# Kernel tuning notes

Measured on AMD Instinct MI355X. Metric: run time of the kernel, lower is better.

Reference implementation:

```python
import jax, jax.numpy as jnp
import numpy as np

BS, N_OPS, N_JOBS, N_MA, E, H = 256, 2000, 50, 40, 128, 128


def setup_inputs() -> dict:
    key = jax.random.key(0)
    ks = jax.random.split(key, 12)
    return {
        "ops_emb": jax.random.normal(ks[0], (BS, N_OPS, E), jnp.float32),
        "ma_emb": jax.random.normal(ks[1], (BS, N_MA, E), jnp.float32),
        "next_op": jax.random.randint(ks[2], (BS, N_JOBS), 0, N_OPS),
        "action_mask": jnp.ones((BS, N_JOBS * N_MA + 1), dtype=bool),
        "dummy": jax.random.normal(ks[3], (2 * E,), jnp.float32),
        "W1": jax.random.normal(ks[4], (2 * E, H), jnp.float32) * 0.05,
        "b1": jax.random.normal(ks[5], (H,), jnp.float32) * 0.05,
        "W2": jax.random.normal(ks[6], (H, H), jnp.float32) * 0.05,
        "b2": jax.random.normal(ks[7], (H,), jnp.float32) * 0.05,
        "W3": jax.random.normal(ks[8], (H, 1), jnp.float32) * 0.05,
        "b3": jax.random.normal(ks[9], (1,), jnp.float32) * 0.05,
    }


def reference(ops_emb, ma_emb, next_op, action_mask, dummy, W1, b1, W2, b2, W3, b3):
    bs, n_ma = ma_emb.shape[:2]
    e = ma_emb.shape[-1]
    # gather_by_index: job_emb [bs, n_jobs, E]
    job_emb = jnp.take_along_axis(ops_emb, next_op[..., None], axis=1)
    # Fused broadcast-concat + first linear: cat(job, ma) @ W1 == job @ W1[:E] + ma @ W1[E:]
    Wj, Wm = W1[:e], W1[e:]
    job_proj = jnp.einsum("bje,eh->bjh", job_emb, Wj)  # [bs, n_jobs, H]
    ma_proj = jnp.einsum("bme,eh->bmh", ma_emb, Wm)    # [bs, n_ma, H]
    h1 = jax.nn.relu(job_proj[:, :, None, :] + ma_proj[:, None, :, :] + b1)  # [bs, nj, nm, H]
    h2 = jax.nn.relu(jnp.einsum("bjmh,hk->bjmk", h1, W2) + b2)
    pair_logits = (jnp.einsum("bjmh,ho->bjmo", h2, W3) + b3)[..., 0]  # [bs, nj, nm]
    pair_logits = pair_logits.reshape(bs, -1)
    # no-op logit from dummy vector through the same MLP
    d1 = jax.nn.relu(dummy @ W1 + b1)
    d2 = jax.nn.relu(d1 @ W2 + b2)
    noop = (d2 @ W3 + b3)  # [1]
    noop = jnp.broadcast_to(noop[None, :], (bs, 1))
    logits = jnp.concatenate([noop, pair_logits], axis=1)  # [bs, nj*nm+1]
    return logits, action_mask
```

## Files before the change

kernel.cpp:

```cpp
#include <hip/hip_runtime.h>
#include <hip/hip_bf16.h>

#define BS_   256
#define NOPS_ 2000
#define NJ_   50
#define NM_   40
#define E_    128
#define H_    128
#define NCOL_ 2001

typedef _Float16 f16;
using f16x8 = __attribute__((ext_vector_type(8))) _Float16;
using f16x4 = __attribute__((ext_vector_type(4))) _Float16;
using f32x4 = __attribute__((ext_vector_type(4))) float;

__global__ __launch_bounds__(512, 2) void fjsp_fused(
    const float* __restrict__ ops_emb,
    const float* __restrict__ ma_emb,
    const int*   __restrict__ next_op,
    const int*   __restrict__ amask,
    const float* __restrict__ dummy,
    const float* __restrict__ W1,
    const float* __restrict__ b1,
    const float* __restrict__ W2,
    const float* __restrict__ b2,
    const float* __restrict__ W3,
    const float* __restrict__ b3,
    float* __restrict__ out)
{
  const int b    = blockIdx.x;
  const int tid  = threadIdx.x;
  const int lane = tid & 63;
  const int wave = tid >> 6;
  const int g    = lane >> 4;
  const int lr   = lane & 15;

  __shared__ __align__(16) f16 Wlds[384][132];
  __shared__ __align__(16) f16 fragL[32 * 64 * 8];
  __shared__ __align__(16) f16 jpL[51][132];
  __shared__ __align__(16) f16 mpL[41][132];

  #pragma unroll 4
  for (int idx = tid; idx < 384 * 32; idx += 512) {
    const int row = idx >> 5, c4 = (idx & 31) * 4;
    const float* src = (row < 256) ? (W1 + (size_t)row * H_ + c4)
                                   : (W2 + (size_t)(row - 256) * H_ + c4);
    const float4 v = *reinterpret_cast<const float4*>(src);
    f16x4 h; h[0] = (f16)v.x; h[1] = (f16)v.y; h[2] = (f16)v.z; h[3] = (f16)v.w;
    *reinterpret_cast<f16x4*>(&Wlds[row][c4]) = h;
  }
  __syncthreads();

  if (wave < 4) {
    const bool isJ   = (wave < 2);
    const int  rbase = isJ ? 0 : 128;
    f16x8 wfr[4][8];
    #pragma unroll
    for (int f = 0; f < 4; ++f) {
      #pragma unroll
      for (int c = 0; c < 8; ++c) {
        f16x8 bb;
        #pragma unroll
        for (int i = 0; i < 8; ++i)
          bb[i] = Wlds[rbase + 32 * f + 8 * g + i][16 * c + lr];
        wfr[f][c] = bb;
      }
    }
    float b1r[8];
    #pragma unroll
    for (int c = 0; c < 8; ++c) b1r[c] = isJ ? 0.f : b1[16 * c + lr];

    const int t0 = (wave == 0) ? 0 : (wave == 1) ? 2 : (wave == 2) ? 0 : 2;
    const int nt = (wave == 3) ? 1 : 2;
    for (int q = 0; q < nt; ++q) {
      const int r0 = (t0 + q) * 16;
      const float* src;
      if (isJ) {
        int jr = r0 + lr; if (jr > 50) jr = 50;
        src = (jr == 50) ? dummy
                         : ops_emb + ((size_t)b * NOPS_ + next_op[b * NJ_ + jr]) * E_;
      } else {
        int mr = r0 + lr; if (mr > 40) mr = 40;
        src = (mr == 40) ? (dummy + E_)
                         : ma_emb + ((size_t)b * NM_ + mr) * E_;
      }
      const float4* ep = reinterpret_cast<const float4*>(src);
      f16x8 af[4];
      #pragma unroll
      for (int f = 0; f < 4; ++f) {
        const float4 v0 = ep[8 * f + 2 * g];
        const float4 v1 = ep[8 * f + 2 * g + 1];
        f16x8 a;
        a[0] = (f16)v0.x; a[1] = (f16)v0.y; a[2] = (f16)v0.z; a[3] = (f16)v0.w;
        a[4] = (f16)v1.x; a[5] = (f16)v1.y; a[6] = (f16)v1.z; a[7] = (f16)v1.w;
        af[f] = a;
      }
      f32x4 acc[8];
      #pragma unroll
      for (int c = 0; c < 8; ++c) acc[c] = f32x4{b1r[c], b1r[c], b1r[c], b1r[c]};
      #pragma unroll
      for (int f = 0; f < 4; ++f)
        #pragma unroll
        for (int c = 0; c < 8; ++c)
          acc[c] = __builtin_amdgcn_mfma_f32_16x16x32_f16(af[f], wfr[f][c], acc[c], 0, 0, 0);
      #pragma unroll
      for (int c = 0; c < 8; ++c) {
        const int col = 16 * c + lr;
        #pragma unroll
        for (int i = 0; i < 4; ++i) {
          const int row = r0 + 4 * g + i;
          if (isJ) { if (row < 51) jpL[row][col] = (f16)acc[c][i]; }
          else     { if (row < 41) mpL[row][col] = (f16)acc[c][i]; }
        }
      }
    }
  } else if (wave < 7) {
    for (int t = wave - 4; t < 32; t += 3) {
      const int f = t >> 3, c = t & 7;
      f16x8 bb;
      #pragma unroll
      for (int i = 0; i < 8; ++i)
        bb[i] = Wlds[256 + 32 * f + 8 * g + i][16 * c + lr];
      *reinterpret_cast<f16x8*>(&fragL[((size_t)t * 64 + lane) * 8]) = bb;
    }
  } else {
    const int* mrow = amask + (size_t)b * NCOL_;
    float* __restrict__ orow = out + (size_t)BS_ * NCOL_ + (size_t)b * NCOL_;
    #pragma unroll 4
    for (int i = lane; i < NCOL_; i += 64) orow[i] = mrow[i] != 0 ? 1.0f : 0.0f;
  }
  __syncthreads();

  f16x8 w2f[4][8];
  #pragma unroll
  for (int f = 0; f < 4; ++f)
    #pragma unroll
    for (int c = 0; c < 8; ++c)
      w2f[f][c] = *reinterpret_cast<const f16x8*>(
          &fragL[((size_t)(f * 8 + c) * 64 + lane) * 8]);
  f16x4 b2h[8];
  float4 w3v[8];
  #pragma unroll
  for (int c = 0; c < 8; ++c) {
    const float4 bv = *reinterpret_cast<const float4*>(b2 + 16 * c + 4 * g);
    f16x4 hh; hh[0] = (f16)bv.x; hh[1] = (f16)bv.y; hh[2] = (f16)bv.z; hh[3] = (f16)bv.w;
    b2h[c] = hh;
    w3v[c] = *reinterpret_cast<const float4*>(W3 + 16 * c + 4 * g);
  }
  const float bias3 = b3[0];
  float* __restrict__ outb = out + (size_t)b * NCOL_;

  #pragma unroll 1
  for (int t = wave; t < 126; t += 8) {
    const int p  = t * 16 + lr;
    const int p2 = (p < 2000) ? p : 2000;
    int j, m;
    if (p2 == 2000) { j = 50; m = 40; }
    else            { j = p2 / 40; m = p2 - j * 40; }
    f16x8 afr[4];
    #pragma unroll
    for (int f = 0; f < 4; ++f) {
      const f16x4 jlo = *reinterpret_cast<const f16x4*>(&jpL[j][32 * f + 8 * g]);
      const f16x4 jhi = *reinterpret_cast<const f16x4*>(&jpL[j][32 * f + 8 * g + 4]);
      const f16x4 mlo = *reinterpret_cast<const f16x4*>(&mpL[m][32 * f + 8 * g]);
      const f16x4 mhi = *reinterpret_cast<const f16x4*>(&mpL[m][32 * f + 8 * g + 4]);
      const f16x4 z   = {(f16)0.f, (f16)0.f, (f16)0.f, (f16)0.f};
      const f16x4 slo = __builtin_elementwise_max(jlo + mlo, z);
      const f16x4 shi = __builtin_elementwise_max(jhi + mhi, z);
      afr[f] = __builtin_shufflevector(slo, shi, 0, 1, 2, 3, 4, 5, 6, 7);
    }
    f32x4 acc[8];
    #pragma unroll
    for (int c = 0; c < 8; ++c)
      acc[c] = f32x4{(float)b2h[c][0], (float)b2h[c][1],
                     (float)b2h[c][2], (float)b2h[c][3]};
    #pragma unroll
    for (int f = 0; f < 4; ++f)
      #pragma unroll
      for (int c = 0; c < 8; ++c)
        acc[c] = __builtin_amdgcn_mfma_f32_16x16x32_f16(w2f[f][c], afr[f], acc[c], 0, 0, 0);
    float pv = 0.f;
    #pragma unroll
    for (int c = 0; c < 8; ++c) {
      pv = fmaf(fmaxf(acc[c][0], 0.f), w3v[c].x, pv);
      pv = fmaf(fmaxf(acc[c][1], 0.f), w3v[c].y, pv);
      pv = fmaf(fmaxf(acc[c][2], 0.f), w3v[c].z, pv);
      pv = fmaf(fmaxf(acc[c][3], 0.f), w3v[c].w, pv);
    }
    pv += __shfl_xor(pv, 16);
    pv += __shfl_xor(pv, 32);
    if (g == 0 && p <= 2000)
      outb[(p == 2000) ? 0 : (p + 1)] = pv + bias3;
  }
}

extern "C" void kernel_launch(void* const* d_in, const int* in_sizes, int n_in,
                              void* d_out, int out_size, void* d_ws, size_t ws_size,
                              hipStream_t stream) {
  (void)in_sizes; (void)n_in; (void)d_ws; (void)ws_size; (void)out_size;
  fjsp_fused<<<dim3(BS_), dim3(512), 0, stream>>>(
      (const float*)d_in[0],
      (const float*)d_in[1],
      (const int*)d_in[2],
      (const int*)d_in[3],
      (const float*)d_in[4],
      (const float*)d_in[5],
      (const float*)d_in[6],
      (const float*)d_in[7],
      (const float*)d_in[8],
      (const float*)d_in[9],
      (const float*)d_in[10],
      (float*)d_out);
}
```

Baseline: 37.43 us.

## Split hidden columns across wave pairs to halve per-wave MFMA register footprint

Each wave now handles only half of the output columns (chalf) in both the layer-1 projections and the layer-2 MLP. This halves the weight-fragment and accumulator registers per wave, and all 8 waves take part in the job projection instead of only two. The two column halves write partial layer-3 dot products to shared memory that reuses the weight buffer, and a final pass sums them, adds the bias and writes the output. This costs an extra __syncthreads and a shared-memory round trip. The mask copy is split across two waves and the jp/mp row padding changes to reduce bank conflicts.

```diff
diff --git a/kernel.cpp b/kernel.cpp
--- a/kernel.cpp
+++ b/kernel.cpp
@@ -34,11 +34,14 @@
   const int wave = tid >> 6;
   const int g    = lane >> 4;
   const int lr   = lane & 15;
-
-  __shared__ __align__(16) f16 Wlds[384][132];
+  const int chalf = wave & 1;
+
+  __shared__ __align__(16) unsigned char SMEM0[384 * 132 * 2];
+  f16 (*Wlds)[132] = reinterpret_cast<f16 (*)[132]>(SMEM0);
+  float* pvpart = reinterpret_cast<float*>(SMEM0);
   __shared__ __align__(16) f16 fragL[32 * 64 * 8];
-  __shared__ __align__(16) f16 jpL[51][132];
-  __shared__ __align__(16) f16 mpL[41][132];
+  __shared__ __align__(16) f16 jpL[51][134];
+  __shared__ __align__(16) f16 mpL[41][134];
 
   #pragma unroll 4
   for (int idx = tid; idx < 384 * 32; idx += 512) {
@@ -51,71 +54,105 @@
   }
   __syncthreads();
 
-  if (wave < 4) {
-    const bool isJ   = (wave < 2);
-    const int  rbase = isJ ? 0 : 128;
-    f16x8 wfr[4][8];
+  {
+    const int jt = wave >> 1;
+    f16x8 wfr[4][4];
+    #pragma unroll
+    for (int f = 0; f < 4; ++f)
+      #pragma unroll
+      for (int cc = 0; cc < 4; ++cc) {
+        const int c = chalf * 4 + cc;
+        f16x8 bb;
+        #pragma unroll
+        for (int i = 0; i < 8; ++i) bb[i] = Wlds[32 * f + 8 * g + i][16 * c + lr];
+        wfr[f][cc] = bb;
+      }
+    int jr = jt * 16 + lr; if (jr > 50) jr = 50;
+    const float* src = (jr == 50)
+        ? dummy
+        : ops_emb + ((size_t)b * NOPS_ + next_op[b * NJ_ + jr]) * E_;
+    const float4* ep = reinterpret_cast<const float4*>(src);
+    f16x8 af[4];
     #pragma unroll
     for (int f = 0; f < 4; ++f) {
-      #pragma unroll
-      for (int c = 0; c < 8; ++c) {
+      const float4 v0 = ep[8 * f + 2 * g];
+      const float4 v1 = ep[8 * f + 2 * g + 1];
+      f16x8 a;
+      a[0] = (f16)v0.x; a[1] = (f16)v0.y; a[2] = (f16)v0.z; a[3] = (f16)v0.w;
+      a[4] = (f16)v1.x; a[5] = (f16)v1.y; a[6] = (f16)v1.z; a[7] = (f16)v1.w;
+      af[f] = a;
+    }
+    f32x4 acc[4];
+    #pragma unroll
+    for (int cc = 0; cc < 4; ++cc) acc[cc] = f32x4{0.f, 0.f, 0.f, 0.f};
+    #pragma unroll
+    for (int f = 0; f < 4; ++f)
+      #pragma unroll
+      for (int cc = 0; cc < 4; ++cc)
+        acc[cc] = __builtin_amdgcn_mfma_f32_16x16x32_f16(af[f], wfr[f][cc], acc[cc], 0, 0, 0);
+    #pragma unroll
+    for (int cc = 0; cc < 4; ++cc) {
+      const int col = 16 * (chalf * 4 + cc) + lr;
+      #pragma unroll
+      for (int i = 0; i < 4; ++i) {
+        const int row = jt * 16 + 4 * g + i;
+        if (row < 51) jpL[row][col] = (f16)acc[cc][i];
+      }
+    }
+  }
+
+  if (wave < 6) {
+    const int mt = wave >> 1;
+    f16x8 wfr[4][4];
+    #pragma unroll
+    for (int f = 0; f < 4; ++f)
+      #pragma unroll
+      for (int cc = 0; cc < 4; ++cc) {
+        const int c = chalf * 4 + cc;
         f16x8 bb;
         #pragma unroll
         for (int i = 0; i < 8; ++i)
-          bb[i] = Wlds[rbase + 32 * f + 8 * g + i][16 * c + lr];
-        wfr[f][c] = bb;
-      }
-    }
-    float b1r[8];
-    #pragma unroll
-    for (int c = 0; c < 8; ++c) b1r[c] = isJ ? 0.f : b1[16 * c + lr];
-
-    const int t0 = (wave == 0) ? 0 : (wave == 1) ? 2 : (wave == 2) ? 0 : 2;
-    const int nt = (wave == 3) ? 1 : 2;
-    for (int q = 0; q < nt; ++q) {
-      const int r0 = (t0 + q) * 16;
-      const float* src;
-      if (isJ) {
-        int jr = r0 + lr; if (jr > 50) jr = 50;
-        src = (jr == 50) ? dummy
-                         : ops_emb + ((size_t)b * NOPS_ + next_op[b * NJ_ + jr]) * E_;
-      } else {
-        int mr = r0 + lr; if (mr > 40) mr = 40;
-        src = (mr == 40) ? (dummy + E_)
-                         : ma_emb + ((size_t)b * NM_ + mr) * E_;
-      }
-      const float4* ep = reinterpret_cast<const float4*>(src);
-      f16x8 af[4];
-      #pragma unroll
-      for (int f = 0; f < 4; ++f) {
-        const float4 v0 = ep[8 * f + 2 * g];
-        const float4 v1 = ep[8 * f + 2 * g + 1];
-        f16x8 a;
-        a[0] = (f16)v0.x; a[1] = (f16)v0.y; a[2] = (f16)v0.z; a[3] = (f16)v0.w;
-        a[4] = (f16)v1.x; a[5] = (f16)v1.y; a[6] = (f16)v1.z; a[7] = (f16)v1.w;
-        af[f] = a;
-      }
-      f32x4 acc[8];
-      #pragma unroll
-      for (int c = 0; c < 8; ++c) acc[c] = f32x4{b1r[c], b1r[c], b1r[c], b1r[c]};
-      #pragma unroll
-      for (int f = 0; f < 4; ++f)
-        #pragma unroll
-        for (int c = 0; c < 8; ++c)
-          acc[c] = __builtin_amdgcn_mfma_f32_16x16x32_f16(af[f], wfr[f][c], acc[c], 0, 0, 0);
-      #pragma unroll
-      for (int c = 0; c < 8; ++c) {
-        const int col = 16 * c + lr;
-        #pragma unroll
-        for (int i = 0; i < 4; ++i) {
-          const int row = r0 + 4 * g + i;
-          if (isJ) { if (row < 51) jpL[row][col] = (f16)acc[c][i]; }
-          else     { if (row < 41) mpL[row][col] = (f16)acc[c][i]; }
-        }
-      }
-    }
-  } else if (wave < 7) {
-    for (int t = wave - 4; t < 32; t += 3) {
+          bb[i] = Wlds[128 + 32 * f + 8 * g + i][16 * c + lr];
+        wfr[f][cc] = bb;
+      }
+    int mr = mt * 16 + lr; if (mr > 40) mr = 40;
+    const float* src = (mr == 40) ? (dummy + E_)
+                                  : ma_emb + ((size_t)b * NM_ + mr) * E_;
+    const float4* ep = reinterpret_cast<const float4*>(src);
+    f16x8 af[4];
+    #pragma unroll
+    for (int f = 0; f < 4; ++f) {
+      const float4 v0 = ep[8 * f + 2 * g];
+      const float4 v1 = ep[8 * f + 2 * g + 1];
+      f16x8 a;
+      a[0] = (f16)v0.x; a[1] = (f16)v0.y; a[2] = (f16)v0.z; a[3] = (f16)v0.w;
+      a[4] = (f16)v1.x; a[5] = (f16)v1.y; a[6] = (f16)v1.z; a[7] = (f16)v1.w;
+      af[f] = a;
+    }
+    f32x4 acc[4];
+    #pragma unroll
+    for (int cc = 0; cc < 4; ++cc) {
+      const float binit = b1[16 * (chalf * 4 + cc) + lr];
+      acc[cc] = f32x4{binit, binit, binit, binit};
+    }
+    #pragma unroll
+    for (int f = 0; f < 4; ++f)
+      #pragma unroll
+      for (int cc = 0; cc < 4; ++cc)
+        acc[cc] = __builtin_amdgcn_mfma_f32_16x16x32_f16(af[f], wfr[f][cc], acc[cc], 0, 0, 0);
+    #pragma unroll
+    for (int cc = 0; cc < 4; ++cc) {
+      const int col = 16 * (chalf * 4 + cc) + lr;
+      #pragma unroll
+      for (int i = 0; i < 4; ++i) {
+        const int row = mt * 16 + 4 * g + i;
+        if (row < 41) mpL[row][col] = (f16)acc[cc][i];
+      }
+    }
+  } else {
+    #pragma unroll 4
+    for (int q = 0; q < 16; ++q) {
+      const int t = (wave - 6) * 16 + q;
       const int f = t >> 3, c = t & 7;
       f16x8 bb;
       #pragma unroll
@@ -123,74 +160,87 @@
         bb[i] = Wlds[256 + 32 * f + 8 * g + i][16 * c + lr];
       *reinterpret_cast<f16x8*>(&fragL[((size_t)t * 64 + lane) * 8]) = bb;
     }
-  } else {
-    const int* mrow = amask + (size_t)b * NCOL_;
-    float* __restrict__ orow = out + (size_t)BS_ * NCOL_ + (size_t)b * NCOL_;
-    #pragma unroll 4
-    for (int i = lane; i < NCOL_; i += 64) orow[i] = mrow[i] != 0 ? 1.0f : 0.0f;
+    const int base  = (wave == 6) ? 0 : 1001;
+    const int count = (wave == 6) ? 1001 : 1000;
+    const int* mrow = amask + (size_t)b * NCOL_ + base;
+    float* __restrict__ orow = out + (size_t)BS_ * NCOL_ + (size_t)b * NCOL_ + base;
+    for (int i = lane; i < count; i += 64) orow[i] = mrow[i] != 0 ? 1.0f : 0.0f;
   }
   __syncthreads();
 
-  f16x8 w2f[4][8];
-  #pragma unroll
-  for (int f = 0; f < 4; ++f)
-    #pragma unroll
-    for (int c = 0; c < 8; ++c)
-      w2f[f][c] = *reinterpret_cast<const f16x8*>(
-          &fragL[((size_t)(f * 8 + c) * 64 + lane) * 8]);
-  f16x4 b2h[8];
-  float4 w3v[8];
-  #pragma unroll
-  for (int c = 0; c < 8; ++c) {
-    const float4 bv = *reinterpret_cast<const float4*>(b2 + 16 * c + 4 * g);
-    f16x4 hh; hh[0] = (f16)bv.x; hh[1] = (f16)bv.y; hh[2] = (f16)bv.z; hh[3] = (f16)bv.w;
-    b2h[c] = hh;
-    w3v[c] = *reinterpret_cast<const float4*>(W3 + 16 * c + 4 * g);
-  }
-  const float bias3 = b3[0];
-  float* __restrict__ outb = out + (size_t)b * NCOL_;
-
-  #pragma unroll 1
-  for (int t = wave; t < 126; t += 8) {
-    const int p  = t * 16 + lr;
-    const int p2 = (p < 2000) ? p : 2000;
-    int j, m;
-    if (p2 == 2000) { j = 50; m = 40; }
-    else            { j = p2 / 40; m = p2 - j * 40; }
-    f16x8 afr[4];
-    #pragma unroll
-    for (int f = 0; f < 4; ++f) {
-      const f16x4 jlo = *reinterpret_cast<const f16x4*>(&jpL[j][32 * f + 8 * g]);
-      const f16x4 jhi = *reinterpret_cast<const f16x4*>(&jpL[j][32 * f + 8 * g + 4]);
-      const f16x4 mlo = *reinterpret_cast<const f16x4*>(&mpL[m][32 * f + 8 * g]);
-      const f16x4 mhi = *reinterpret_cast<const f16x4*>(&mpL[m][32 * f + 8 * g + 4]);
-      const f16x4 z   = {(f16)0.f, (f16)0.f, (f16)0.f, (f16)0.f};
-      const f16x4 slo = __builtin_elementwise_max(jlo + mlo, z);
-      const f16x4 shi = __builtin_elementwise_max(jhi + mhi, z);
-      afr[f] = __builtin_shufflevector(slo, shi, 0, 1, 2, 3, 4, 5, 6, 7);
-    }
-    f32x4 acc[8];
-    #pragma unroll
-    for (int c = 0; c < 8; ++c)
-      acc[c] = f32x4{(float)b2h[c][0], (float)b2h[c][1],
-                     (float)b2h[c][2], (float)b2h[c][3]};
-    #pragma unroll
-    for (int f = 0; f < 4; ++f)
-      #pragma unroll
-      for (int c = 0; c < 8; ++c)
-        acc[c] = __builtin_amdgcn_mfma_f32_16x16x32_f16(w2f[f][c], afr[f], acc[c], 0, 0, 0);
-    float pv = 0.f;
-    #pragma unroll
-    for (int c = 0; c < 8; ++c) {
-      pv = fmaf(fmaxf(acc[c][0], 0.f), w3v[c].x, pv);
-      pv = fmaf(fmaxf(acc[c][1], 0.f), w3v[c].y, pv);
-      pv = fmaf(fmaxf(acc[c][2], 0.f), w3v[c].z, pv);
-      pv = fmaf(fmaxf(acc[c][3], 0.f), w3v[c].w, pv);
-    }
-    pv += __shfl_xor(pv, 16);
-    pv += __shfl_xor(pv, 32);
-    if (g == 0 && p <= 2000)
-      outb[(p == 2000) ? 0 : (p + 1)] = pv + bias3;
+  {
+    const int gp = wave >> 1;
+    f16x8 w2f[4][4];
+    #pragma unroll
+    for (int f = 0; f < 4; ++f)
+      #pragma unroll
+      for (int cc = 0; cc < 4; ++cc)
+        w2f[f][cc] = *reinterpret_cast<const f16x8*>(
+            &fragL[((size_t)(f * 8 + chalf * 4 + cc) * 64 + lane) * 8]);
+    f16x4 b2h[4];
+    float4 w3v[4];
+    #pragma unroll
+    for (int cc = 0; cc < 4; ++cc) {
+      const int c = chalf * 4 + cc;
+      const float4 bv = *reinterpret_cast<const float4*>(b2 + 16 * c + 4 * g);
+      f16x4 hh; hh[0] = (f16)bv.x; hh[1] = (f16)bv.y; hh[2] = (f16)bv.z; hh[3] = (f16)bv.w;
+      b2h[cc] = hh;
+      w3v[cc] = *reinterpret_cast<const float4*>(W3 + 16 * c + 4 * g);
+    }
+    float* pvp = pvpart + chalf * 2016;
+
+    #pragma unroll 1
+    for (int t = gp; t < 126; t += 4) {
+      const int p  = t * 16 + lr;
+      const int p2 = (p < 2000) ? p : 2000;
+      int j, m;
+      if (p2 == 2000) { j = 50; m = 40; }
+      else            { j = p2 / 40; m = p2 - j * 40; }
+      f32x4 acc[4];
+      #pragma unroll
+      for (int cc = 0; cc < 4; ++cc)
+        acc[cc] = f32x4{(float)b2h[cc][0], (float)b2h[cc][1],
+                        (float)b2h[cc][2], (float)b2h[cc][3]};
+      #pragma unroll
+      for (int f = 0; f < 4; ++f) {
+        const f16x4 jlo = *reinterpret_cast<const f16x4*>(&jpL[j][32 * f + 8 * g]);
+        const f16x4 jhi = *reinterpret_cast<const f16x4*>(&jpL[j][32 * f + 8 * g + 4]);
+        const f16x4 mlo = *reinterpret_cast<const f16x4*>(&mpL[m][32 * f + 8 * g]);
+        const f16x4 mhi = *reinterpret_cast<const f16x4*>(&mpL[m][32 * f + 8 * g + 4]);
+        const f16x4 z   = {(f16)0.f, (f16)0.f, (f16)0.f, (f16)0.f};
+        const f16x4 slo = __builtin_elementwise_max(jlo + mlo, z);
+        const f16x4 shi = __builtin_elementwise_max(jhi + mhi, z);
+        const f16x8 afr = __builtin_shufflevector(slo, shi, 0, 1, 2, 3, 4, 5, 6, 7);
+        #pragma unroll
+        for (int cc = 0; cc < 4; ++cc)
+          acc[cc] = __builtin_amdgcn_mfma_f32_16x16x32_f16(w2f[f][cc], afr, acc[cc], 0, 0, 0);
+      }
+      float pv = 0.f;
+      #pragma unroll
+      for (int cc = 0; cc < 4; ++cc) {
+        pv = fmaf(fmaxf(acc[cc][0], 0.f), w3v[cc].x, pv);
+        pv = fmaf(fmaxf(acc[cc][1], 0.f), w3v[cc].y, pv);
+        pv = fmaf(fmaxf(acc[cc][2], 0.f), w3v[cc].z, pv);
+        pv = fmaf(fmaxf(acc[cc][3], 0.f), w3v[cc].w, pv);
+      }
+      pv += __shfl_xor(pv, 16);
+      pv += __shfl_xor(pv, 32);
+      if (g == 0) pvp[p] = pv;
+    }
+  }
+  __syncthreads();
+
+  {
+    const float bias3 = b3[0];
+    float* __restrict__ outb = out + (size_t)b * NCOL_;
+    #pragma unroll
+    for (int q = 0; q < 4; ++q) {
+      const int p = tid + q * 512;
+      if (p <= 2000) {
+        const float v = pvpart[p] + pvpart[2016 + p] + bias3;
+        outb[(p == 2000) ? 0 : (p + 1)] = v;
+      }
+    }
   }
 }
 
```

New measurement: 37.47 us. About the same (+0.1%).
